# Kernel tuning notes

Hardware: AMD Instinct MI355X
Metric: run time of the kernel (lower is better)

## Reference

```python
import jax, jax.numpy as jnp
import numpy as np

B, P, C, NOBJ = 64, 24564, 81, 16
THRESHOLD = 0.5
NEG_POS_RATIO = 3
ALPHA = 1.0


def cxcy_to_xy(cxcy):
    # (cx, cy, w, h) -> (x_min, y_min, x_max, y_max)
    return jnp.concatenate([cxcy[..., :2] - cxcy[..., 2:] / 2,
                            cxcy[..., :2] + cxcy[..., 2:] / 2], axis=-1)


def xy_to_cxcy(xy):
    return jnp.concatenate([(xy[..., :2] + xy[..., 2:]) / 2,
                            xy[..., 2:] - xy[..., :2]], axis=-1)


def cxcy_to_gcxgcy(cxcy, priors_cxcy):
    # SSD encoding with variances (10, 5)
    g_cxcy = (cxcy[..., :2] - priors_cxcy[..., :2]) / (priors_cxcy[..., 2:] / 10.0)
    g_wh = jnp.log(cxcy[..., 2:] / priors_cxcy[..., 2:]) * 5.0
    return jnp.concatenate([g_cxcy, g_wh], axis=-1)


def find_jaccard_overlap(set1, set2):
    # set1: [n1, 4] xy, set2: [n2, 4] xy -> IoU [n1, n2]
    lo = jnp.maximum(set1[:, None, :2], set2[None, :, :2])
    hi = jnp.minimum(set1[:, None, 2:], set2[None, :, 2:])
    inter = jnp.prod(jnp.clip(hi - lo, 0.0), axis=-1)
    area1 = jnp.prod(set1[:, 2:] - set1[:, :2], axis=-1)
    area2 = jnp.prod(set2[:, 2:] - set2[:, :2], axis=-1)
    union = area1[:, None] + area2[None, :] - inter
    return inter / union


def setup_inputs() -> dict:
    key = jax.random.key(0)
    k1, k2, k3, k4, k5, k6, k7 = jax.random.split(key, 7)
    predicted_locs = jax.random.normal(k1, (B, P, 4), dtype=jnp.float32)
    predicted_scores = jax.random.normal(k2, (B, P, C), dtype=jnp.float32)
    # valid ground-truth boxes in boundary coords, built from center/size
    ctr = jax.random.uniform(k3, (B, NOBJ, 2), minval=0.2, maxval=0.8)
    wh = jax.random.uniform(k4, (B, NOBJ, 2), minval=0.05, maxval=0.3)
    boxes = jnp.concatenate([ctr - wh / 2, ctr + wh / 2], axis=-1).astype(jnp.float32)
    labels = jax.random.randint(k5, (B, NOBJ), 1, C)  # 0 is background
    pc = jax.random.uniform(k6, (P, 2), minval=0.0, maxval=1.0)
    pwh = jax.random.uniform(k7, (P, 2), minval=0.05, maxval=0.5)
    priors_cxcy = jnp.concatenate([pc, pwh], axis=-1).astype(jnp.float32)
    return {"predicted_locs": predicted_locs, "predicted_scores": predicted_scores,
            "boxes": boxes, "labels": labels, "priors_cxcy": priors_cxcy}


def reference(predicted_locs, predicted_scores, boxes, labels, priors_cxcy):
    priors_xy = cxcy_to_xy(priors_cxcy)

    def match_one(bx, lb):
        # bx: [NOBJ, 4] xy, lb: [NOBJ]
        overlap = find_jaccard_overlap(bx, priors_xy)        # [NOBJ, P]
        ov_per_prior = overlap.max(axis=0)                   # [P]
        obj_per_prior = overlap.argmax(axis=0)               # [P]
        prior_per_obj = overlap.argmax(axis=1)               # [NOBJ]
        # force each object to match its best prior
        obj_per_prior = obj_per_prior.at[prior_per_obj].set(jnp.arange(NOBJ))
        ov_per_prior = ov_per_prior.at[prior_per_obj].set(1.0)
        lab = lb[obj_per_prior]                              # [P]
        lab = jnp.where(ov_per_prior < THRESHOLD, 0, lab)
        tl = cxcy_to_gcxgcy(xy_to_cxcy(bx[obj_per_prior]), priors_cxcy)  # [P, 4]
        return tl, lab

    true_locs, true_classes = jax.vmap(match_one)(boxes, labels)  # [B,P,4], [B,P]

    pos = true_classes != 0                                   # [B, P]
    n_pos = pos.sum(axis=1)                                   # [B]
    total_pos = pos.sum()

    # smooth-L1 (beta=1) over positive priors, mean over elements
    diff = predicted_locs - true_locs
    ad = jnp.abs(diff)
    sl1 = jnp.where(ad < 1.0, 0.5 * diff * diff, ad - 0.5)    # [B, P, 4]
    loc_loss = (sl1 * pos[..., None]).sum() / (total_pos.astype(jnp.float32) * 4.0)

    # per-prior cross-entropy
    logp = jax.nn.log_softmax(predicted_scores, axis=-1)      # [B, P, C]
    ce = -jnp.take_along_axis(logp, true_classes[..., None], axis=-1)[..., 0]  # [B, P]

    conf_loss_pos = jnp.sum(ce * pos)
    conf_loss_neg = jnp.where(pos, 0.0, ce)
    neg_sorted = -jnp.sort(-conf_loss_neg, axis=1)            # descending per image
    ranks = jnp.arange(P)[None, :]
    hard = ranks < (NEG_POS_RATIO * n_pos)[:, None]
    conf_loss_hard_neg = jnp.sum(neg_sorted * hard)

    conf_loss = (conf_loss_hard_neg + conf_loss_pos) / total_pos.astype(jnp.float32)
    return conf_loss + ALPHA * loc_loss
```

## Files before the change

kernel.cpp:

```cpp
#include <hip/hip_runtime.h>
#include <cstdint>
#include <cstddef>

#define B_      64
#define P_      24564
#define C_      81
#define NOBJ_   16
#define SLICE_  1536
#define NCEB_   6141
#define CHUNKS_ 96
#define NBLK_   6144
#define TILE_F  2592

__device__ __forceinline__ float smooth_l1(float d){
  float ad = fabsf(d);
  return (ad < 1.0f) ? 0.5f * d * d : ad - 0.5f;
}

__device__ __forceinline__ void stage_tile(const float* gsrc, float* lds, int lane){
  const float4* s4 = reinterpret_cast<const float4*>(gsrc);
  #pragma unroll
  for (int k = 0; k < 10; ++k){
    __builtin_amdgcn_global_load_lds(
        (const __attribute__((address_space(1))) void*)(s4 + k * 64 + lane),
        (__attribute__((address_space(3))) void*)(lds + k * 256), 16, 0, 0);
  }
  if (lane < 8)
    __builtin_amdgcn_global_load_lds(
        (const __attribute__((address_space(1))) void*)(s4 + 640 + lane),
        (__attribute__((address_space(3))) void*)(lds + 2560), 16, 0, 0);
}

__device__ __forceinline__ void tile_compute(const float* lbuf, int t, int lane,
                                             size_t row0, float* __restrict__ ce0){
  const int r = lane & 31, h = lane >> 5;
  const int base = r * 81 + h * 41;
  float sum = 0.f;
  #pragma unroll
  for (int j = 0; j < 40; ++j) sum += __expf(lbuf[base + j]);
  if (!h) sum += __expf(lbuf[base + 40]);
  sum += __shfl_xor(sum, 32);
  if (!h)
    ce0[row0 + (size_t)t * 32 + r] = __logf(sum) - lbuf[r * 81];
}

__global__ __launch_bounds__(64) void k_main(const float* __restrict__ scores,
                                             const float* __restrict__ priors,
                                             const float* __restrict__ boxes,
                                             float* __restrict__ ce0,
                                             unsigned long long* __restrict__ ppbest,
                                             unsigned long long* __restrict__ pob){
  __shared__ float sM[2 * TILE_F];
  const int lane = threadIdx.x;
  const int blk  = blockIdx.x;

  const int img = blk / CHUNKS_;
  const int chk = blk - img * CHUNKS_;
  const int pr0 = chk * 256;
  const int nval = P_ - pr0;

  float4 prv[4]; bool pvd[4];
  #pragma unroll
  for (int j = 0; j < 4; ++j){
    int idx = j * 64 + lane;
    pvd[j] = idx < nval;
    prv[j] = reinterpret_cast<const float4*>(priors)[pr0 + (pvd[j] ? idx : 0)];
  }

  const bool ce_act = blk < NCEB_;
  const size_t row0 = (size_t)blk * 256;
  const float* g0 = scores + row0 * (size_t)C_;
  if (ce_act) stage_tile(g0, sM, lane);

  float px0[4], py0[4], px1[4], py1[4], pa[4];
  #pragma unroll
  for (int j = 0; j < 4; ++j){
    px0[j] = prv[j].x - prv[j].z * 0.5f;  py0[j] = prv[j].y - prv[j].w * 0.5f;
    px1[j] = prv[j].x + prv[j].z * 0.5f;  py1[j] = prv[j].y + prv[j].w * 0.5f;
    pa[j]  = (px1[j] - px0[j]) * (py1[j] - py0[j]);
  }
  float mx[4]; int am[4];
  #pragma unroll
  for (int j = 0; j < 4; ++j){ mx[j] = -1.f; am[j] = 0; }

  #pragma unroll
  for (int o = 0; o < NOBJ_; ++o){
    float4 bo = reinterpret_cast<const float4*>(boxes)[img * NOBJ_ + o];
    float ba = (bo.z - bo.x) * (bo.w - bo.y);
    float bbv = -1.f; int bbi = 0x7FFFFFFF;
    #pragma unroll
    for (int j = 0; j < 4; ++j){
      float ix = fminf(bo.z, px1[j]) - fmaxf(bo.x, px0[j]);
      float iy = fminf(bo.w, py1[j]) - fmaxf(bo.y, py0[j]);
      ix = fmaxf(ix, 0.f); iy = fmaxf(iy, 0.f);
      float inter = ix * iy;
      float v = __fdividef(inter, ba + pa[j] - inter);
      if (!pvd[j]) v = -2.f;
      int p = pr0 + j * 64 + lane;
      if (v > bbv){ bbv = v; bbi = p; }
      if (v > mx[j]){ mx[j] = v; am[j] = o; }
    }
    #pragma unroll
    for (int off = 32; off; off >>= 1){
      float v2 = __shfl_down(bbv, off);
      int   i2 = __shfl_down(bbi, off);
      if (v2 > bbv || (v2 == bbv && i2 < bbi)){ bbv = v2; bbi = i2; }
    }
    if (lane == 0)
      pob[(size_t)blk * NOBJ_ + o] =
          ((unsigned long long)__float_as_uint(bbv) << 32)
        | (unsigned long long)(0xFFFFFFFFu - (unsigned)bbi);
  }
  #pragma unroll
  for (int j = 0; j < 4; ++j){
    if (pvd[j])
      ppbest[(size_t)img * P_ + pr0 + j * 64 + lane] =
          ((unsigned long long)__float_as_uint(mx[j]) << 32) | (unsigned)am[j];
  }

  if (!ce_act) return;

  stage_tile(g0 + TILE_F, sM + TILE_F, lane);
  int buf = 0;
  for (int t = 0; t < 6; ++t){
    asm volatile("s_waitcnt vmcnt(11)" ::: "memory");
    tile_compute(sM + buf * TILE_F, t, lane, row0, ce0);
    stage_tile(g0 + (size_t)(t + 2) * TILE_F, sM + buf * TILE_F, lane);
    buf ^= 1;
  }
  asm volatile("s_waitcnt vmcnt(11)" ::: "memory");
  tile_compute(sM + buf * TILE_F, 6, lane, row0, ce0);
  buf ^= 1;
  asm volatile("s_waitcnt vmcnt(0)" ::: "memory");
  tile_compute(sM + buf * TILE_F, 7, lane, row0, ce0);
}

__global__ __launch_bounds__(256) void k_fixup(const float* __restrict__ boxes,
                                               const int*   __restrict__ labels,
                                               const float* __restrict__ priors,
                                               const float* __restrict__ pred_locs,
                                               const float* __restrict__ scores,
                                               const unsigned long long* __restrict__ pob,
                                               const unsigned long long* __restrict__ ppbest,
                                               const float* __restrict__ ce0,
                                               float* __restrict__ ce_neg,
                                               int*   __restrict__ npos_p,
                                               float* __restrict__ sl1_p,
                                               float* __restrict__ cpos_p){
  const int b = blockIdx.x, slice = blockIdx.y, tid = threadIdx.x;
  __shared__ float sb[NOBJ_ * 4];
  __shared__ int   slab[NOBJ_];
  __shared__ int   sppo[NOBJ_];
  __shared__ unsigned long long pm[16][NOBJ_];
  if (tid < NOBJ_ * 4) sb[tid] = boxes[b * NOBJ_ * 4 + tid];
  if (tid < NOBJ_) slab[tid] = labels[b * NOBJ_ + tid];
  {
    int o = tid & 15, g = tid >> 4;
    unsigned long long m = 0ull;
    for (int c = g * 6; c < g * 6 + 6; ++c){
      unsigned long long e = pob[(size_t)(b * CHUNKS_ + c) * NOBJ_ + o];
      if (e > m) m = e;
    }
    pm[g][o] = m;
  }
  __syncthreads();
  if (tid < NOBJ_){
    unsigned long long m = 0ull;
    #pragma unroll
    for (int g = 0; g < 16; ++g) if (pm[g][tid] > m) m = pm[g][tid];
    sppo[tid] = (int)(0xFFFFFFFFu - (unsigned)(m & 0xFFFFFFFFull));
  }
  __syncthreads();

  int cnt = 0; float sl1 = 0.f, cpos = 0.f;
  const int p0 = slice * SLICE_;
  for (int k = 0; k < SLICE_ / 256; ++k){
    int p = p0 + k * 256 + tid;
    if (p < P_){
      const size_t row = (size_t)b * P_ + p;
      unsigned long long e = ppbest[row];
      float mxv = __uint_as_float((unsigned)(e >> 32));
      int   am  = (int)(e & 0xFFFFFFFFull);
      #pragma unroll
      for (int o = 0; o < NOBJ_; ++o){
        if (sppo[o] == p){ am = o; mxv = 1.0f; }
      }
      int lab = slab[am];
      if (mxv < 0.5f) lab = 0;
      float c0 = ce0[row];
      float negv;
      if (lab != 0){
        ++cnt; negv = 0.f;
        float4 pr = reinterpret_cast<const float4*>(priors)[p];
        float x0 = sb[am*4+0], y0 = sb[am*4+1], x1 = sb[am*4+2], y1 = sb[am*4+3];
        float cx = (x0 + x1) / 2.f, cy = (y0 + y1) / 2.f;
        float w_ = x1 - x0, h_ = y1 - y0;
        float g0 = (cx - pr.x) / (pr.z / 10.0f);
        float g1 = (cy - pr.y) / (pr.w / 10.0f);
        float g2 = logf(w_ / pr.z) * 5.0f;
        float g3 = logf(h_ / pr.w) * 5.0f;
        float4 pl = reinterpret_cast<const float4*>(pred_locs)[row];
        sl1 += smooth_l1(pl.x - g0) + smooth_l1(pl.y - g1)
             + smooth_l1(pl.z - g2) + smooth_l1(pl.w - g3);
        const float* srow = scores + row * (size_t)C_;
        cpos += c0 + srow[0] - srow[lab];
      } else {
        negv = fmaxf(c0, 0.f);
      }
      ce_neg[row] = negv;
    }
  }
  for (int off = 32; off; off >>= 1){
    cnt  += __shfl_down(cnt, off);
    sl1  += __shfl_down(sl1, off);
    cpos += __shfl_down(cpos, off);
  }
  __shared__ int   rc[4];
  __shared__ float rs[4], rp[4];
  const int lane = tid & 63, wid = tid >> 6;
  if (lane == 0){ rc[wid] = cnt; rs[wid] = sl1; rp[wid] = cpos; }
  __syncthreads();
  if (tid == 0){
    int c = 0; float s = 0.f, q = 0.f;
    for (int w = 0; w < 4; ++w){ c += rc[w]; s += rs[w]; q += rp[w]; }
    npos_p[b * 16 + slice] = c;
    sl1_p[b * 16 + slice]  = s;
    cpos_p[b * 16 + slice] = q;
  }
}

__global__ __launch_bounds__(512) void k_topk(const float* __restrict__ ce_neg,
                                              const int*   __restrict__ npos_p,
                                              float* __restrict__ hard){
  const int b = blockIdx.x, tid = threadIdx.x;
  const float* v = ce_neg + (size_t)b * P_;

  __shared__ int sKs;
  if (tid == 0){
    int k = 0;
    #pragma unroll
    for (int s = 0; s < 16; ++s) k += npos_p[b * 16 + s];
    sKs = 3 * k;
  }
  __syncthreads();
  const int K = sKs;
  if (K <= 0){ if (tid == 0) hard[b] = 0.f; return; }

  __shared__ int hist[32 * 257];
  __shared__ int histT[256];
  __shared__ unsigned s_prefix;
  __shared__ int s_rem;
  __shared__ float rsum[8];
  const int lane = tid & 63, wid = tid >> 6;
  const int copy = tid & 31;

  if (K >= P_){
    float s = 0.f;
    for (int p = tid; p < P_; p += 512) s += v[p];
    #pragma unroll
    for (int off = 32; off; off >>= 1) s += __shfl_down(s, off);
    if (lane == 0) rsum[wid] = s;
    __syncthreads();
    if (tid == 0){
      float t = 0.f;
      for (int w = 0; w < 8; ++w) t += rsum[w];
      hard[b] = t;
    }
    return;
  }

  unsigned prefix = 0; int remaining = K;
  for (int shift = 24; shift >= 0; shift -= 8){
    for (int i = tid; i < 32 * 257; i += 512) hist[i] = 0;
    __syncthreads();
    unsigned hmask = (shift == 24) ? 0u : (0xFFFFFFFFu << (shift + 8));
    for (int p = tid; p < P_; p += 512){
      unsigned u = __float_as_uint(v[p]);
      if ((u & hmask) == prefix) atomicAdd(&hist[copy * 257 + ((u >> shift) & 255)], 1);
    }
    __syncthreads();
    if (tid < 256){
      int s = 0;
      #pragma unroll
      for (int w = 0; w < 32; ++w) s += hist[w * 257 + tid];
      histT[tid] = s;
    }
    __syncthreads();
    if (wid == 0){
      int a0 = histT[lane*4+0], a1 = histT[lane*4+1],
          a2 = histT[lane*4+2], a3 = histT[lane*4+3];
      int tl = a0 + a1 + a2 + a3;
      int run = tl;
      #pragma unroll
      for (int off = 1; off < 64; off <<= 1){
        int x = __shfl_down(run, off);
        if (lane + off < 64) run += x;
      }
      int E  = run - tl;
      int s3 = E;
      int s2 = s3 + a3;
      int s1 = s2 + a2;
      int s0 = s1 + a1;
      if (s0 < remaining && s0 + a0 >= remaining){ s_prefix = prefix | ((unsigned)(lane*4+0) << shift); s_rem = remaining - s0; }
      if (s1 < remaining && s1 + a1 >= remaining){ s_prefix = prefix | ((unsigned)(lane*4+1) << shift); s_rem = remaining - s1; }
      if (s2 < remaining && s2 + a2 >= remaining){ s_prefix = prefix | ((unsigned)(lane*4+2) << shift); s_rem = remaining - s2; }
      if (s3 < remaining && s3 + a3 >= remaining){ s_prefix = prefix | ((unsigned)(lane*4+3) << shift); s_rem = remaining - s3; }
    }
    __syncthreads();
    prefix = s_prefix;
    remaining = s_rem;
    __syncthreads();
  }

  float tv = __uint_as_float(prefix);
  float sgt = 0.f;
  for (int p = tid; p < P_; p += 512){
    unsigned u = __float_as_uint(v[p]);
    if (u > prefix) sgt += v[p];
  }
  #pragma unroll
  for (int off = 32; off; off >>= 1) sgt += __shfl_down(sgt, off);
  if (lane == 0) rsum[wid] = sgt;
  __syncthreads();
  if (tid == 0){
    float s = 0.f;
    for (int w = 0; w < 8; ++w) s += rsum[w];
    hard[b] = s + (float)remaining * tv;
  }
}

__global__ __launch_bounds__(1024) void k_final(const float* __restrict__ cpos_p,
                                                const float* __restrict__ sl1_p,
                                                const int*   __restrict__ npos_p,
                                                const float* __restrict__ hard,
                                                float* __restrict__ out){
  const int tid = threadIdx.x, lane = tid & 63, wid = tid >> 6;
  float cp = cpos_p[tid];
  float sl = sl1_p[tid];
  int   np = npos_p[tid];
  float hd = (tid < B_) ? hard[tid] : 0.f;

  #pragma unroll
  for (int off = 32; off; off >>= 1){
    cp += __shfl_down(cp, off);
    sl += __shfl_down(sl, off);
    np += __shfl_down(np, off);
    hd += __shfl_down(hd, off);
  }
  __shared__ float rcp[16], rsl[16], rhd[16];
  __shared__ int   rnp[16];
  if (lane == 0){ rcp[wid] = cp; rsl[wid] = sl; rnp[wid] = np; rhd[wid] = hd; }
  __syncthreads();
  if (tid == 0){
    float tcp = 0.f, tsl = 0.f, thd = 0.f; int tnp = 0;
    for (int w = 0; w < 16; ++w){ tcp += rcp[w]; tsl += rsl[w]; tnp += rnp[w]; thd += rhd[w]; }
    float tp = (float)tnp;
    out[0] = (thd + tcp) / tp + tsl / (tp * 4.0f);
  }
}

extern "C" void kernel_launch(void* const* d_in, const int* in_sizes, int n_in,
                              void* d_out, int out_size, void* d_ws, size_t ws_size,
                              hipStream_t stream){
  const float* pred_locs = (const float*)d_in[0];
  const float* scores    = (const float*)d_in[1];
  const float* boxes     = (const float*)d_in[2];
  const int*   labels    = (const int*)d_in[3];
  const float* priors    = (const float*)d_in[4];

  const size_t BP = (size_t)B_ * P_;
  char* w = (char*)d_ws;
  float* ce_neg = (float*)w;
  float* ce0    = (float*)(w + BP * 4);
  unsigned long long* ppbest = (unsigned long long*)(w + 2 * BP * 4);
  unsigned long long* pob    = (unsigned long long*)(w + 2 * BP * 4 + BP * 8);
  char*  w2 = w + 2 * BP * 4 + BP * 8 + (size_t)NBLK_ * NOBJ_ * 8;
  int*   npos_p = (int*)  w2;
  float* sl1_p  = (float*)(w2 + 1024 * 4);
  float* cpos_p = (float*)(w2 + 1024 * 8);
  float* hard   = (float*)(w2 + 1024 * 12);

  k_main<<<NBLK_, 64, 0, stream>>>(scores, priors, boxes, ce0, ppbest, pob);

  dim3 g2(B_, 16);
  k_fixup<<<g2, 256, 0, stream>>>(boxes, labels, priors, pred_locs, scores,
                                  pob, ppbest, ce0, ce_neg, npos_p, sl1_p, cpos_p);

  k_topk<<<B_, 512, 0, stream>>>(ce_neg, npos_p, hard);

  k_final<<<1, 1024, 0, stream>>>(cpos_p, sl1_p, npos_p, hard, (float*)d_out);
}
```

Baseline: 200.3 us.

## Fuse matching, CE and loss partials into main kernel; merge fixup/topk/final into tail

The main kernel now does per-image chunked work. Alongside the IoU matching it computes log-sum-exp, the positive/negative CE, smooth-L1 and per-chunk partial sums directly from LDS-staged score tiles. This removes the ce0 and ppbest intermediates and the separate fixup pass that re-read them. A single tail kernel per image applies the forced best-prior-per-object corrections, runs the top-k hard negative selection, and finishes the global reduction with a last-block atomic counter. The trade-offs are fewer launches and less global traffic, against smaller tiles with more pipeline steps and extra correction logic for forced matches.

```diff
diff --git a/kernel.cpp b/kernel.cpp
--- a/kernel.cpp
+++ b/kernel.cpp
@@ -6,58 +6,87 @@
 #define P_      24564
 #define C_      81
 #define NOBJ_   16
-#define SLICE_  1536
-#define NCEB_   6141
 #define CHUNKS_ 96
 #define NBLK_   6144
-#define TILE_F  2592
+#define TILE_F  1296
+#define TILE_F4 324
+
+typedef unsigned long long u64;
 
 __device__ __forceinline__ float smooth_l1(float d){
   float ad = fabsf(d);
   return (ad < 1.0f) ? 0.5f * d * d : ad - 0.5f;
 }
 
-__device__ __forceinline__ void stage_tile(const float* gsrc, float* lds, int lane){
-  const float4* s4 = reinterpret_cast<const float4*>(gsrc);
-  #pragma unroll
-  for (int k = 0; k < 10; ++k){
-    __builtin_amdgcn_global_load_lds(
-        (const __attribute__((address_space(1))) void*)(s4 + k * 64 + lane),
-        (__attribute__((address_space(3))) void*)(lds + k * 256), 16, 0, 0);
-  }
-  if (lane < 8)
-    __builtin_amdgcn_global_load_lds(
-        (const __attribute__((address_space(1))) void*)(s4 + 640 + lane),
-        (__attribute__((address_space(3))) void*)(lds + 2560), 16, 0, 0);
-}
-
-__device__ __forceinline__ void tile_compute(const float* lbuf, int t, int lane,
-                                             size_t row0, float* __restrict__ ce0){
-  const int r = lane & 31, h = lane >> 5;
-  const int base = r * 81 + h * 41;
-  float sum = 0.f;
-  #pragma unroll
-  for (int j = 0; j < 40; ++j) sum += __expf(lbuf[base + j]);
-  if (!h) sum += __expf(lbuf[base + 40]);
-  sum += __shfl_xor(sum, 32);
-  if (!h)
-    ce0[row0 + (size_t)t * 32 + r] = __logf(sum) - lbuf[r * 81];
+__device__ __forceinline__ float iou_pb(float bx0, float by0, float bx1, float by1,
+                                        float ba, float px0, float py0,
+                                        float px1, float py1, float pa){
+  float ix = fminf(bx1, px1) - fmaxf(bx0, px0);
+  float iy = fminf(by1, py1) - fmaxf(by0, py0);
+  ix = fmaxf(ix, 0.f); iy = fmaxf(iy, 0.f);
+  float inter = ix * iy;
+  return __fdividef(inter, ba + pa - inter);
+}
+
+__device__ __forceinline__ float sl1_row4(const float* sbox, int am, float4 pr, float4 pl){
+  float x0 = sbox[am*4+0], y0 = sbox[am*4+1], x1 = sbox[am*4+2], y1 = sbox[am*4+3];
+  float cx = (x0 + x1) / 2.f, cy = (y0 + y1) / 2.f;
+  float w_ = x1 - x0, h_ = y1 - y0;
+  float g0 = (cx - pr.x) / (pr.z / 10.0f);
+  float g1 = (cy - pr.y) / (pr.w / 10.0f);
+  float g2 = logf(w_ / pr.z) * 5.0f;
+  float g3 = logf(h_ / pr.w) * 5.0f;
+  return smooth_l1(pl.x - g0) + smooth_l1(pl.y - g1)
+       + smooth_l1(pl.z - g2) + smooth_l1(pl.w - g3);
 }
 
 __global__ __launch_bounds__(64) void k_main(const float* __restrict__ scores,
                                              const float* __restrict__ priors,
                                              const float* __restrict__ boxes,
-                                             float* __restrict__ ce0,
-                                             unsigned long long* __restrict__ ppbest,
-                                             unsigned long long* __restrict__ pob){
+                                             const int*   __restrict__ labels,
+                                             const float* __restrict__ pred_locs,
+                                             float* __restrict__ ce_neg,
+                                             u64*   __restrict__ pob,
+                                             int*   __restrict__ npos_c,
+                                             float* __restrict__ sl1_c,
+                                             float* __restrict__ cpos_c,
+                                             int*   __restrict__ done){
   __shared__ float sM[2 * TILE_F];
+  __shared__ float lmx[256];
+  __shared__ int   lam[256];
+  __shared__ float sbox[NOBJ_ * 4];
+  __shared__ int   slab[NOBJ_];
   const int lane = threadIdx.x;
-  const int blk  = blockIdx.x;
-
-  const int img = blk / CHUNKS_;
-  const int chk = blk - img * CHUNKS_;
-  const int pr0 = chk * 256;
-  const int nval = P_ - pr0;
+  const int chk = blockIdx.x, img = blockIdx.y;
+  const int blkid = img * CHUNKS_ + chk;
+  if (blkid == 0 && lane == 0) *done = 0;
+
+  const int pr0  = chk * 256;
+  const int nval = min(256, P_ - pr0);
+  sbox[lane] = boxes[img * NOBJ_ * 4 + lane];
+  if (lane < NOBJ_) slab[lane] = labels[img * NOBJ_ + lane];
+
+  const size_t brow = (size_t)img * P_ + pr0;
+  const float4* g4 = reinterpret_cast<const float4*>(scores + brow * (size_t)C_);
+  const int lim = (int)(((size_t)B_ * P_ - brow) * C_ / 4) - 1;
+
+  auto STAGE = [&](int t, float* dst){
+    const int b4 = t * TILE_F4;
+    #pragma unroll
+    for (int k = 0; k < 5; ++k){
+      int idx = min(b4 + k * 64 + lane, lim);
+      __builtin_amdgcn_global_load_lds(
+          (const __attribute__((address_space(1))) void*)(g4 + idx),
+          (__attribute__((address_space(3))) void*)(dst + k * 256), 16, 0, 0);
+    }
+    int idx = min(b4 + 320 + lane, lim);
+    if (lane < 4)
+      __builtin_amdgcn_global_load_lds(
+          (const __attribute__((address_space(1))) void*)(g4 + idx),
+          (__attribute__((address_space(3))) void*)(dst + 1280), 16, 0, 0);
+  };
+
+  STAGE(0, sM);
 
   float4 prv[4]; bool pvd[4];
   #pragma unroll
@@ -66,12 +95,6 @@
     pvd[j] = idx < nval;
     prv[j] = reinterpret_cast<const float4*>(priors)[pr0 + (pvd[j] ? idx : 0)];
   }
-
-  const bool ce_act = blk < NCEB_;
-  const size_t row0 = (size_t)blk * 256;
-  const float* g0 = scores + row0 * (size_t)C_;
-  if (ce_act) stage_tile(g0, sM, lane);
-
   float px0[4], py0[4], px1[4], py1[4], pa[4];
   #pragma unroll
   for (int j = 0; j < 4; ++j){
@@ -85,16 +108,12 @@
 
   #pragma unroll
   for (int o = 0; o < NOBJ_; ++o){
-    float4 bo = reinterpret_cast<const float4*>(boxes)[img * NOBJ_ + o];
-    float ba = (bo.z - bo.x) * (bo.w - bo.y);
+    float bx0 = sbox[o*4+0], by0 = sbox[o*4+1], bx1 = sbox[o*4+2], by1 = sbox[o*4+3];
+    float ba = (bx1 - bx0) * (by1 - by0);
     float bbv = -1.f; int bbi = 0x7FFFFFFF;
     #pragma unroll
     for (int j = 0; j < 4; ++j){
-      float ix = fminf(bo.z, px1[j]) - fmaxf(bo.x, px0[j]);
-      float iy = fminf(bo.w, py1[j]) - fmaxf(bo.y, py0[j]);
-      ix = fmaxf(ix, 0.f); iy = fmaxf(iy, 0.f);
-      float inter = ix * iy;
-      float v = __fdividef(inter, ba + pa[j] - inter);
+      float v = iou_pb(bx0, by0, bx1, by1, ba, px0[j], py0[j], px1[j], py1[j], pa[j]);
       if (!pvd[j]) v = -2.f;
       int p = pr0 + j * 64 + lane;
       if (v > bbv){ bbv = v; bbi = p; }
@@ -107,255 +126,294 @@
       if (v2 > bbv || (v2 == bbv && i2 < bbi)){ bbv = v2; bbi = i2; }
     }
     if (lane == 0)
-      pob[(size_t)blk * NOBJ_ + o] =
-          ((unsigned long long)__float_as_uint(bbv) << 32)
-        | (unsigned long long)(0xFFFFFFFFu - (unsigned)bbi);
-  }
-  #pragma unroll
-  for (int j = 0; j < 4; ++j){
-    if (pvd[j])
-      ppbest[(size_t)img * P_ + pr0 + j * 64 + lane] =
-          ((unsigned long long)__float_as_uint(mx[j]) << 32) | (unsigned)am[j];
-  }
-
-  if (!ce_act) return;
-
-  stage_tile(g0 + TILE_F, sM + TILE_F, lane);
-  int buf = 0;
-  for (int t = 0; t < 6; ++t){
-    asm volatile("s_waitcnt vmcnt(11)" ::: "memory");
-    tile_compute(sM + buf * TILE_F, t, lane, row0, ce0);
-    stage_tile(g0 + (size_t)(t + 2) * TILE_F, sM + buf * TILE_F, lane);
-    buf ^= 1;
-  }
-  asm volatile("s_waitcnt vmcnt(11)" ::: "memory");
-  tile_compute(sM + buf * TILE_F, 6, lane, row0, ce0);
-  buf ^= 1;
+      pob[(size_t)blkid * NOBJ_ + o] =
+          ((u64)__float_as_uint(bbv) << 32) | (u64)(0xFFFFFFFFu - (unsigned)bbi);
+  }
+  #pragma unroll
+  for (int j = 0; j < 4; ++j){ lmx[j*64 + lane] = mx[j]; lam[j*64 + lane] = am[j]; }
+
+  int cnt = 0; float sl1 = 0.f, cpos = 0.f;
+  const int rr = lane & 15, h = lane >> 4;
+  const int rbase = rr * 81 + (h == 0 ? 0 : 1 + 20 * h);
+
+  auto COMPUTE = [&](int t){
+    const float* lb = sM + (t & 1) * TILE_F;
+    float sa = 0.f, sb = 0.f;
+    #pragma unroll
+    for (int j = 0; j < 10; ++j){
+      sa += __expf(lb[rbase + 2*j]);
+      sb += __expf(lb[rbase + 2*j + 1]);
+    }
+    if (h == 0) sa += __expf(lb[rbase + 20]);
+    float sum = sa + sb;
+    sum += __shfl_xor(sum, 16);
+    sum += __shfl_xor(sum, 32);
+    if (h == 0){
+      int pl_ = t * 16 + rr;
+      if (pl_ < nval){
+        size_t row = brow + pl_;
+        float lse = __logf(sum);
+        float s0  = lb[rr * 81];
+        bool pos = lmx[pl_] >= 0.5f;
+        ce_neg[row] = pos ? 0.f : fmaxf(lse - s0, 0.f);
+        if (pos){
+          int a = lam[pl_];
+          int lb2 = slab[a];
+          cpos += lse - lb[rr * 81 + lb2];
+          ++cnt;
+          float4 pr  = reinterpret_cast<const float4*>(priors)[pr0 + pl_];
+          float4 pl4 = reinterpret_cast<const float4*>(pred_locs)[row];
+          sl1 += sl1_row4(sbox, a, pr, pl4);
+        }
+      }
+    }
+  };
+
+  for (int t = 0; t < 15; ++t){
+    STAGE(t + 1, sM + ((t + 1) & 1) * TILE_F);
+    asm volatile("s_waitcnt vmcnt(6)" ::: "memory");
+    COMPUTE(t);
+  }
   asm volatile("s_waitcnt vmcnt(0)" ::: "memory");
-  tile_compute(sM + buf * TILE_F, 7, lane, row0, ce0);
-}
-
-__global__ __launch_bounds__(256) void k_fixup(const float* __restrict__ boxes,
-                                               const int*   __restrict__ labels,
-                                               const float* __restrict__ priors,
-                                               const float* __restrict__ pred_locs,
-                                               const float* __restrict__ scores,
-                                               const unsigned long long* __restrict__ pob,
-                                               const unsigned long long* __restrict__ ppbest,
-                                               const float* __restrict__ ce0,
-                                               float* __restrict__ ce_neg,
-                                               int*   __restrict__ npos_p,
-                                               float* __restrict__ sl1_p,
-                                               float* __restrict__ cpos_p){
-  const int b = blockIdx.x, slice = blockIdx.y, tid = threadIdx.x;
-  __shared__ float sb[NOBJ_ * 4];
-  __shared__ int   slab[NOBJ_];
-  __shared__ int   sppo[NOBJ_];
-  __shared__ unsigned long long pm[16][NOBJ_];
-  if (tid < NOBJ_ * 4) sb[tid] = boxes[b * NOBJ_ * 4 + tid];
-  if (tid < NOBJ_) slab[tid] = labels[b * NOBJ_ + tid];
-  {
-    int o = tid & 15, g = tid >> 4;
-    unsigned long long m = 0ull;
-    for (int c = g * 6; c < g * 6 + 6; ++c){
-      unsigned long long e = pob[(size_t)(b * CHUNKS_ + c) * NOBJ_ + o];
-      if (e > m) m = e;
-    }
-    pm[g][o] = m;
-  }
-  __syncthreads();
-  if (tid < NOBJ_){
-    unsigned long long m = 0ull;
-    #pragma unroll
-    for (int g = 0; g < 16; ++g) if (pm[g][tid] > m) m = pm[g][tid];
-    sppo[tid] = (int)(0xFFFFFFFFu - (unsigned)(m & 0xFFFFFFFFull));
-  }
-  __syncthreads();
-
-  int cnt = 0; float sl1 = 0.f, cpos = 0.f;
-  const int p0 = slice * SLICE_;
-  for (int k = 0; k < SLICE_ / 256; ++k){
-    int p = p0 + k * 256 + tid;
-    if (p < P_){
-      const size_t row = (size_t)b * P_ + p;
-      unsigned long long e = ppbest[row];
-      float mxv = __uint_as_float((unsigned)(e >> 32));
-      int   am  = (int)(e & 0xFFFFFFFFull);
-      #pragma unroll
-      for (int o = 0; o < NOBJ_; ++o){
-        if (sppo[o] == p){ am = o; mxv = 1.0f; }
-      }
-      int lab = slab[am];
-      if (mxv < 0.5f) lab = 0;
-      float c0 = ce0[row];
-      float negv;
-      if (lab != 0){
-        ++cnt; negv = 0.f;
-        float4 pr = reinterpret_cast<const float4*>(priors)[p];
-        float x0 = sb[am*4+0], y0 = sb[am*4+1], x1 = sb[am*4+2], y1 = sb[am*4+3];
-        float cx = (x0 + x1) / 2.f, cy = (y0 + y1) / 2.f;
-        float w_ = x1 - x0, h_ = y1 - y0;
-        float g0 = (cx - pr.x) / (pr.z / 10.0f);
-        float g1 = (cy - pr.y) / (pr.w / 10.0f);
-        float g2 = logf(w_ / pr.z) * 5.0f;
-        float g3 = logf(h_ / pr.w) * 5.0f;
-        float4 pl = reinterpret_cast<const float4*>(pred_locs)[row];
-        sl1 += smooth_l1(pl.x - g0) + smooth_l1(pl.y - g1)
-             + smooth_l1(pl.z - g2) + smooth_l1(pl.w - g3);
-        const float* srow = scores + row * (size_t)C_;
-        cpos += c0 + srow[0] - srow[lab];
-      } else {
-        negv = fmaxf(c0, 0.f);
-      }
-      ce_neg[row] = negv;
-    }
-  }
-  for (int off = 32; off; off >>= 1){
+  COMPUTE(15);
+
+  #pragma unroll
+  for (int off = 8; off; off >>= 1){
     cnt  += __shfl_down(cnt, off);
     sl1  += __shfl_down(sl1, off);
     cpos += __shfl_down(cpos, off);
   }
-  __shared__ int   rc[4];
-  __shared__ float rs[4], rp[4];
+  if (lane == 0){
+    npos_c[blkid] = cnt; sl1_c[blkid] = sl1; cpos_c[blkid] = cpos;
+  }
+}
+
+__global__ __launch_bounds__(1024) void k_tail(const float* __restrict__ scores,
+                                               const float* __restrict__ priors,
+                                               const float* __restrict__ boxes,
+                                               const int*   __restrict__ labels,
+                                               const float* __restrict__ pred_locs,
+                                               const u64*   __restrict__ pob,
+                                               const int*   __restrict__ npos_c,
+                                               const float* __restrict__ sl1_c,
+                                               const float* __restrict__ cpos_c,
+                                               float* __restrict__ ce_neg,
+                                               int*   __restrict__ npos_img,
+                                               float* __restrict__ sl1_img,
+                                               float* __restrict__ cpos_img,
+                                               float* __restrict__ hard_img,
+                                               int*   __restrict__ done,
+                                               float* __restrict__ out){
+  const int img = blockIdx.x, tid = threadIdx.x;
   const int lane = tid & 63, wid = tid >> 6;
-  if (lane == 0){ rc[wid] = cnt; rs[wid] = sl1; rp[wid] = cpos; }
+  __shared__ u64   pm[64][NOBJ_];
+  __shared__ int   sppo[NOBJ_];
+  __shared__ float sbox[NOBJ_ * 4];
+  __shared__ int   slab[NOBJ_];
+  __shared__ float sredA[96], sredB[96];
+  __shared__ int   sredI[96];
+  __shared__ int   s_npos;
+  __shared__ float s_sl1, s_cpos, s_hard;
+  __shared__ int   s_last;
+
+  if (tid < 64) sbox[tid] = boxes[img * 64 + tid];
+  if (tid < 16) slab[tid] = labels[img * 16 + tid];
+  {
+    int o = tid & 15, g = tid >> 4;
+    u64 m = pob[(size_t)(img * CHUNKS_ + g) * NOBJ_ + o];
+    if (g < 32){
+      u64 e = pob[(size_t)(img * CHUNKS_ + 64 + g) * NOBJ_ + o];
+      if (e > m) m = e;
+    }
+    pm[g][o] = m;
+  }
+  if (tid < 96){
+    sredI[tid] = npos_c[img * CHUNKS_ + tid];
+    sredA[tid] = sl1_c[img * CHUNKS_ + tid];
+    sredB[tid] = cpos_c[img * CHUNKS_ + tid];
+  }
   __syncthreads();
+  if (tid < 16){
+    u64 m = pm[0][tid];
+    for (int g = 1; g < 64; ++g) if (pm[g][tid] > m) m = pm[g][tid];
+    sppo[tid] = (int)(0xFFFFFFFFu - (unsigned)(m & 0xFFFFFFFFull));
+  }
   if (tid == 0){
     int c = 0; float s = 0.f, q = 0.f;
-    for (int w = 0; w < 4; ++w){ c += rc[w]; s += rs[w]; q += rp[w]; }
-    npos_p[b * 16 + slice] = c;
-    sl1_p[b * 16 + slice]  = s;
-    cpos_p[b * 16 + slice] = q;
-  }
-}
-
-__global__ __launch_bounds__(512) void k_topk(const float* __restrict__ ce_neg,
-                                              const int*   __restrict__ npos_p,
-                                              float* __restrict__ hard){
-  const int b = blockIdx.x, tid = threadIdx.x;
-  const float* v = ce_neg + (size_t)b * P_;
-
-  __shared__ int sKs;
-  if (tid == 0){
-    int k = 0;
-    #pragma unroll
-    for (int s = 0; s < 16; ++s) k += npos_p[b * 16 + s];
-    sKs = 3 * k;
+    for (int i = 0; i < 96; ++i){ c += sredI[i]; s += sredA[i]; q += sredB[i]; }
+    s_npos = c; s_sl1 = s; s_cpos = q;
   }
   __syncthreads();
-  const int K = sKs;
-  if (K <= 0){ if (tid == 0) hard[b] = 0.f; return; }
-
+
+  int npd = 0; float sld = 0.f, cpd = 0.f;
+  if (wid == 0 && lane < 16){
+    int o = lane, p = sppo[o];
+    bool is_last = true;
+    for (int o2 = o + 1; o2 < 16; ++o2) if (sppo[o2] == p) is_last = false;
+    if (is_last){
+      float4 pr = reinterpret_cast<const float4*>(priors)[p];
+      float px0 = pr.x - pr.z * 0.5f, py0 = pr.y - pr.w * 0.5f;
+      float px1 = pr.x + pr.z * 0.5f, py1 = pr.y + pr.w * 0.5f;
+      float pa  = (px1 - px0) * (py1 - py0);
+      float mxo = -1.f; int amo = 0;
+      for (int oo = 0; oo < 16; ++oo){
+        float bx0 = sbox[oo*4+0], by0 = sbox[oo*4+1],
+              bx1 = sbox[oo*4+2], by1 = sbox[oo*4+3];
+        float ba = (bx1 - bx0) * (by1 - by0);
+        float v = iou_pb(bx0, by0, bx1, by1, ba, px0, py0, px1, py1, pa);
+        if (v > mxo){ mxo = v; amo = oo; }
+      }
+      bool pos_old = mxo >= 0.5f;
+      size_t row = (size_t)img * P_ + p;
+      float4 pl4 = reinterpret_cast<const float4*>(pred_locs)[row];
+      float sl_new = sl1_row4(sbox, o, pr, pl4);
+      int lab_new = slab[o];
+      float s_new = scores[row * (size_t)C_ + lab_new];
+      if (pos_old){
+        float sl_old = sl1_row4(sbox, amo, pr, pl4);
+        float s_old  = scores[row * (size_t)C_ + slab[amo]];
+        sld = sl_new - sl_old;
+        cpd = s_old - s_new;
+      } else {
+        npd = 1;
+        float ce0v = ce_neg[row];
+        float s0   = scores[row * (size_t)C_];
+        sld = sl_new;
+        cpd = ce0v + s0 - s_new;
+        ce_neg[row] = 0.f;
+      }
+    }
+  }
+  if (wid == 0){
+    #pragma unroll
+    for (int off = 8; off; off >>= 1){
+      npd += __shfl_down(npd, off);
+      sld += __shfl_down(sld, off);
+      cpd += __shfl_down(cpd, off);
+    }
+    if (lane == 0){
+      s_npos += npd; s_sl1 += sld; s_cpos += cpd;
+      npos_img[img] = s_npos; sl1_img[img] = s_sl1; cpos_img[img] = s_cpos;
+    }
+  }
+  __threadfence();
+  __syncthreads();
+
+  const int K = 3 * s_npos;
+  const float* v = ce_neg + (size_t)img * P_;
   __shared__ int hist[32 * 257];
   __shared__ int histT[256];
   __shared__ unsigned s_prefix;
   __shared__ int s_rem;
-  __shared__ float rsum[8];
-  const int lane = tid & 63, wid = tid >> 6;
+  __shared__ float rsum[16];
   const int copy = tid & 31;
 
-  if (K >= P_){
+  if (K <= 0){
+    if (tid == 0) s_hard = 0.f;
+    __syncthreads();
+  } else if (K >= P_){
     float s = 0.f;
-    for (int p = tid; p < P_; p += 512) s += v[p];
+    for (int p = tid; p < P_; p += 1024) s += v[p];
     #pragma unroll
     for (int off = 32; off; off >>= 1) s += __shfl_down(s, off);
     if (lane == 0) rsum[wid] = s;
     __syncthreads();
     if (tid == 0){
       float t = 0.f;
-      for (int w = 0; w < 8; ++w) t += rsum[w];
-      hard[b] = t;
-    }
-    return;
-  }
-
-  unsigned prefix = 0; int remaining = K;
-  for (int shift = 24; shift >= 0; shift -= 8){
-    for (int i = tid; i < 32 * 257; i += 512) hist[i] = 0;
-    __syncthreads();
-    unsigned hmask = (shift == 24) ? 0u : (0xFFFFFFFFu << (shift + 8));
-    for (int p = tid; p < P_; p += 512){
+      for (int w = 0; w < 16; ++w) t += rsum[w];
+      s_hard = t;
+    }
+    __syncthreads();
+  } else {
+    unsigned prefix = 0; int remaining = K;
+    for (int shift = 24; shift >= 0; shift -= 8){
+      for (int i = tid; i < 32 * 257; i += 1024) hist[i] = 0;
+      __syncthreads();
+      unsigned hmask = (shift == 24) ? 0u : (0xFFFFFFFFu << (shift + 8));
+      for (int p = tid; p < P_; p += 1024){
+        unsigned u = __float_as_uint(v[p]);
+        if ((u & hmask) == prefix) atomicAdd(&hist[copy * 257 + ((u >> shift) & 255)], 1);
+      }
+      __syncthreads();
+      if (tid < 256){
+        int s = 0;
+        #pragma unroll
+        for (int w = 0; w < 32; ++w) s += hist[w * 257 + tid];
+        histT[tid] = s;
+      }
+      __syncthreads();
+      if (wid == 0){
+        int a0 = histT[lane*4+0], a1 = histT[lane*4+1],
+            a2 = histT[lane*4+2], a3 = histT[lane*4+3];
+        int tl = a0 + a1 + a2 + a3;
+        int run = tl;
+        #pragma unroll
+        for (int off = 1; off < 64; off <<= 1){
+          int x = __shfl_down(run, off);
+          if (lane + off < 64) run += x;
+        }
+        int E  = run - tl;
+        int s3 = E;
+        int s2 = s3 + a3;
+        int s1 = s2 + a2;
+        int s0 = s1 + a1;
+        if (s0 < remaining && s0 + a0 >= remaining){ s_prefix = prefix | ((unsigned)(lane*4+0) << shift); s_rem = remaining - s0; }
+        if (s1 < remaining && s1 + a1 >= remaining){ s_prefix = prefix | ((unsigned)(lane*4+1) << shift); s_rem = remaining - s1; }
+        if (s2 < remaining && s2 + a2 >= remaining){ s_prefix = prefix | ((unsigned)(lane*4+2) << shift); s_rem = remaining - s2; }
+        if (s3 < remaining && s3 + a3 >= remaining){ s_prefix = prefix | ((unsigned)(lane*4+3) << shift); s_rem = remaining - s3; }
+      }
+      __syncthreads();
+      prefix = s_prefix;
+      remaining = s_rem;
+      __syncthreads();
+    }
+    float tv = __uint_as_float(prefix);
+    float sgt = 0.f;
+    for (int p = tid; p < P_; p += 1024){
       unsigned u = __float_as_uint(v[p]);
-      if ((u & hmask) == prefix) atomicAdd(&hist[copy * 257 + ((u >> shift) & 255)], 1);
-    }
-    __syncthreads();
-    if (tid < 256){
-      int s = 0;
+      if (u > prefix) sgt += v[p];
+    }
+    #pragma unroll
+    for (int off = 32; off; off >>= 1) sgt += __shfl_down(sgt, off);
+    if (lane == 0) rsum[wid] = sgt;
+    __syncthreads();
+    if (tid == 0){
+      float s = 0.f;
+      for (int w = 0; w < 16; ++w) s += rsum[w];
+      s_hard = s + (float)remaining * tv;
+    }
+    __syncthreads();
+  }
+
+  if (tid == 0){
+    hard_img[img] = s_hard;
+    __threadfence();
+    int old = atomicAdd(done, 1);
+    s_last = (old == B_ - 1) ? 1 : 0;
+  }
+  __syncthreads();
+  if (s_last){
+    if (tid == 0) __threadfence();
+    __syncthreads();
+    float np = 0.f, sl = 0.f, cp = 0.f, hd = 0.f;
+    if (tid < 64){
+      np = (float)__hip_atomic_load(&npos_img[tid], __ATOMIC_RELAXED, __HIP_MEMORY_SCOPE_AGENT);
+      sl = __hip_atomic_load(&sl1_img[tid],  __ATOMIC_RELAXED, __HIP_MEMORY_SCOPE_AGENT);
+      cp = __hip_atomic_load(&cpos_img[tid], __ATOMIC_RELAXED, __HIP_MEMORY_SCOPE_AGENT);
+      hd = __hip_atomic_load(&hard_img[tid], __ATOMIC_RELAXED, __HIP_MEMORY_SCOPE_AGENT);
+    }
+    if (wid == 0){
       #pragma unroll
-      for (int w = 0; w < 32; ++w) s += hist[w * 257 + tid];
-      histT[tid] = s;
-    }
-    __syncthreads();
-    if (wid == 0){
-      int a0 = histT[lane*4+0], a1 = histT[lane*4+1],
-          a2 = histT[lane*4+2], a3 = histT[lane*4+3];
-      int tl = a0 + a1 + a2 + a3;
-      int run = tl;
-      #pragma unroll
-      for (int off = 1; off < 64; off <<= 1){
-        int x = __shfl_down(run, off);
-        if (lane + off < 64) run += x;
-      }
-      int E  = run - tl;
-      int s3 = E;
-      int s2 = s3 + a3;
-      int s1 = s2 + a2;
-      int s0 = s1 + a1;
-      if (s0 < remaining && s0 + a0 >= remaining){ s_prefix = prefix | ((unsigned)(lane*4+0) << shift); s_rem = remaining - s0; }
-      if (s1 < remaining && s1 + a1 >= remaining){ s_prefix = prefix | ((unsigned)(lane*4+1) << shift); s_rem = remaining - s1; }
-      if (s2 < remaining && s2 + a2 >= remaining){ s_prefix = prefix | ((unsigned)(lane*4+2) << shift); s_rem = remaining - s2; }
-      if (s3 < remaining && s3 + a3 >= remaining){ s_prefix = prefix | ((unsigned)(lane*4+3) << shift); s_rem = remaining - s3; }
-    }
-    __syncthreads();
-    prefix = s_prefix;
-    remaining = s_rem;
-    __syncthreads();
-  }
-
-  float tv = __uint_as_float(prefix);
-  float sgt = 0.f;
-  for (int p = tid; p < P_; p += 512){
-    unsigned u = __float_as_uint(v[p]);
-    if (u > prefix) sgt += v[p];
-  }
-  #pragma unroll
-  for (int off = 32; off; off >>= 1) sgt += __shfl_down(sgt, off);
-  if (lane == 0) rsum[wid] = sgt;
-  __syncthreads();
-  if (tid == 0){
-    float s = 0.f;
-    for (int w = 0; w < 8; ++w) s += rsum[w];
-    hard[b] = s + (float)remaining * tv;
-  }
-}
-
-__global__ __launch_bounds__(1024) void k_final(const float* __restrict__ cpos_p,
-                                                const float* __restrict__ sl1_p,
-                                                const int*   __restrict__ npos_p,
-                                                const float* __restrict__ hard,
-                                                float* __restrict__ out){
-  const int tid = threadIdx.x, lane = tid & 63, wid = tid >> 6;
-  float cp = cpos_p[tid];
-  float sl = sl1_p[tid];
-  int   np = npos_p[tid];
-  float hd = (tid < B_) ? hard[tid] : 0.f;
-
-  #pragma unroll
-  for (int off = 32; off; off >>= 1){
-    cp += __shfl_down(cp, off);
-    sl += __shfl_down(sl, off);
-    np += __shfl_down(np, off);
-    hd += __shfl_down(hd, off);
-  }
-  __shared__ float rcp[16], rsl[16], rhd[16];
-  __shared__ int   rnp[16];
-  if (lane == 0){ rcp[wid] = cp; rsl[wid] = sl; rnp[wid] = np; rhd[wid] = hd; }
-  __syncthreads();
-  if (tid == 0){
-    float tcp = 0.f, tsl = 0.f, thd = 0.f; int tnp = 0;
-    for (int w = 0; w < 16; ++w){ tcp += rcp[w]; tsl += rsl[w]; tnp += rnp[w]; thd += rhd[w]; }
-    float tp = (float)tnp;
-    out[0] = (thd + tcp) / tp + tsl / (tp * 4.0f);
+      for (int off = 32; off; off >>= 1){
+        np += __shfl_down(np, off);
+        sl += __shfl_down(sl, off);
+        cp += __shfl_down(cp, off);
+        hd += __shfl_down(hd, off);
+      }
+      if (lane == 0){
+        out[0] = (hd + cp) / np + sl / (np * 4.0f);
+      }
+    }
   }
 }
 
@@ -371,22 +429,24 @@
   const size_t BP = (size_t)B_ * P_;
   char* w = (char*)d_ws;
   float* ce_neg = (float*)w;
-  float* ce0    = (float*)(w + BP * 4);
-  unsigned long long* ppbest = (unsigned long long*)(w + 2 * BP * 4);
-  unsigned long long* pob    = (unsigned long long*)(w + 2 * BP * 4 + BP * 8);
-  char*  w2 = w + 2 * BP * 4 + BP * 8 + (size_t)NBLK_ * NOBJ_ * 8;
-  int*   npos_p = (int*)  w2;
-  float* sl1_p  = (float*)(w2 + 1024 * 4);
-  float* cpos_p = (float*)(w2 + 1024 * 8);
-  float* hard   = (float*)(w2 + 1024 * 12);
-
-  k_main<<<NBLK_, 64, 0, stream>>>(scores, priors, boxes, ce0, ppbest, pob);
-
-  dim3 g2(B_, 16);
-  k_fixup<<<g2, 256, 0, stream>>>(boxes, labels, priors, pred_locs, scores,
-                                  pob, ppbest, ce0, ce_neg, npos_p, sl1_p, cpos_p);
-
-  k_topk<<<B_, 512, 0, stream>>>(ce_neg, npos_p, hard);
-
-  k_final<<<1, 1024, 0, stream>>>(cpos_p, sl1_p, npos_p, hard, (float*)d_out);
-}
+  u64*   pob    = (u64*)(w + BP * 4);
+  char*  w2 = w + BP * 4 + (size_t)NBLK_ * NOBJ_ * 8;
+  int*   npos_c = (int*)  w2;
+  float* sl1_c  = (float*)(w2 + NBLK_ * 4);
+  float* cpos_c = (float*)(w2 + NBLK_ * 8);
+  char*  w3 = w2 + NBLK_ * 12;
+  int*   npos_img = (int*)  w3;
+  float* sl1_img  = (float*)(w3 + 256);
+  float* cpos_img = (float*)(w3 + 512);
+  float* hard_img = (float*)(w3 + 768);
+  int*   done     = (int*)  (w3 + 1024);
+
+  dim3 g1(CHUNKS_, B_);
+  k_main<<<g1, 64, 0, stream>>>(scores, priors, boxes, labels, pred_locs,
+                                ce_neg, pob, npos_c, sl1_c, cpos_c, done);
+
+  k_tail<<<B_, 1024, 0, stream>>>(scores, priors, boxes, labels, pred_locs,
+                                  pob, npos_c, sl1_c, cpos_c, ce_neg,
+                                  npos_img, sl1_img, cpos_img, hard_img,
+                                  done, (float*)d_out);
+}
```

Result: faster. 182.6 us (-8.8%).
